# Performance work log

Hardware: AMD Instinct MI355X
Metric: run time of the kernel (lower is better)

## Reference

```python
import jax, jax.numpy as jnp
import numpy as np

N = 150000      # active voxels
C = 64          # head input channels
KK = 9          # 3x3 kernel offsets
H = W = 700     # BEV feature map
BN_EPS = 1e-5
HEADS = [("heatmap", 3), ("center", 2), ("center_z", 1), ("dim", 3), ("rot", 2)]


def _build_neighbor_table(seed=0):
    """Submanifold 3x3 neighbor indices for N active voxels on an HxW grid.
    Entry -1 means the neighbor site is inactive (contributes zero)."""
    rng = np.random.default_rng(seed)
    flat = rng.choice(H * W, size=N, replace=False)
    ys, xs = flat // W, flat % W
    lut = np.full(H * W, -1, np.int64)
    lut[flat] = np.arange(N)
    nbr = np.full((N, KK), -1, np.int64)
    k = 0
    for dy in (-1, 0, 1):
        for dx in (-1, 0, 1):
            ny, nx = ys + dy, xs + dx
            valid = (ny >= 0) & (ny < H) & (nx >= 0) & (nx < W)
            nf = np.where(valid, ny * W + nx, 0)
            nbr[:, k] = np.where(valid, lut[nf], -1)
            k += 1
    return nbr


def setup_inputs() -> dict:
    key = jax.random.key(0)
    ks = jax.random.split(key, 2 + 2 * len(HEADS))
    inp = {
        "features": jax.random.normal(ks[0], (N, C), jnp.float32),
        "nbr_idx": jnp.asarray(_build_neighbor_table(), jnp.int32),
        # one 3x3 subm conv per head, stacked: [n_heads, 9, C_in, C_out]
        "W3": jax.random.normal(ks[1], (len(HEADS), KK, C, C), jnp.float32) * 0.05,
        "gamma": jnp.ones((len(HEADS), C), jnp.float32),
        "beta": jnp.zeros((len(HEADS), C), jnp.float32),
    }
    for i, (name, oc) in enumerate(HEADS):
        inp[f"W1_{name}"] = jax.random.normal(ks[2 + i], (C, oc), jnp.float32) * 0.001
        if name == "heatmap":
            inp[f"b1_{name}"] = jnp.full((oc,), -float(np.log((1 - 0.01) / 0.01)), jnp.float32)
        else:
            inp[f"b1_{name}"] = jnp.zeros((oc,), jnp.float32)
    return inp


def _forward(features, nbr_idx, W3, gamma, beta, W1s, b1s):
    valid = nbr_idx >= 0                                  # [N, 9]
    idx = jnp.where(valid, nbr_idx, 0)
    # gather active-neighbor features; missing neighbors -> zero (subm conv)
    gathered = features[idx] * valid[..., None].astype(features.dtype)  # [N, 9, C]
    # all heads share the same input sparse tensor -> batched gather-GEMM
    h = jnp.einsum('nkc,hkco->hno', gathered, W3)         # [n_heads, N, C]
    # BatchNorm1d (training-mode batch stats, biased var) + ReLU
    mean = h.mean(axis=1, keepdims=True)
    var = ((h - mean) ** 2).mean(axis=1, keepdims=True)
    hn = (h - mean) * jax.lax.rsqrt(var + BN_EPS)
    hn = jax.nn.relu(hn * gamma[:, None, :] + beta[:, None, :])
    # per-head 1x1 subm conv == linear on active features
    return tuple(hn[i] @ W1s[i] + b1s[i] for i in range(len(HEADS)))


def reference(features, nbr_idx, W3, gamma, beta,
              W1_heatmap, b1_heatmap, W1_center, b1_center,
              W1_center_z, b1_center_z, W1_dim, b1_dim, W1_rot, b1_rot):
    W1s = [W1_heatmap, W1_center, W1_center_z, W1_dim, W1_rot]
    b1s = [b1_heatmap, b1_center, b1_center_z, b1_dim, b1_rot]
    return _forward(features, nbr_idx, W3, gamma, beta, W1s, b1s)
```

## Files before the change

### kernel.cpp

```cpp
#include <hip/hip_runtime.h>

#define NVOX 150000
#define BM 128
#define MTILES 1172
#define SROW 150016
#define NCOL 320

typedef __attribute__((ext_vector_type(8))) short bf16x8;
typedef __attribute__((ext_vector_type(4))) float f32x4;

__device__ __forceinline__ unsigned short f2bf(float f) {
    unsigned u = __builtin_bit_cast(unsigned, f);
    u += 0x7fffu + ((u >> 16) & 1u);
    return (unsigned short)(u >> 16);
}

__device__ __forceinline__ void gld16(const void* g, void* l) {
    __builtin_amdgcn_global_load_lds(
        (const __attribute__((address_space(1))) unsigned int*)g,
        (__attribute__((address_space(3))) unsigned int*)l, 16, 0, 0);
}

__global__ void prep_feat(const float* __restrict__ src, unsigned short* __restrict__ dst) {
    int i = blockIdx.x * 256 + threadIdx.x;
    if (i < NVOX * 64) dst[i] = f2bf(src[i]);
    else if (i < NVOX * 64 + 64) dst[i] = 0;
}

__global__ void prep_w3(const float* __restrict__ w3, unsigned short* __restrict__ bt,
                        float* __restrict__ stats) {
    int i = blockIdx.x * 256 + threadIdx.x;
    int h = i / 36864;
    int rem = i - h * 36864;
    int kk = rem >> 12;
    int c = (rem >> 6) & 63;
    int o = rem & 63;
    bt[(size_t)(((h * 9 + kk) * 8) + (c >> 3)) * 512 + o * 8 + (c & 7)] = f2bf(w3[i]);
    if (i < 2 * NCOL) stats[i] = 0.f;
}

__global__ __launch_bounds__(256, 4)
void gemm_kernel(const unsigned short* __restrict__ featB,
                 const unsigned short* __restrict__ Bt2,
                 const int* __restrict__ nbr,
                 unsigned short* __restrict__ hbuf,
                 float* __restrict__ stats) {
    __shared__ __align__(16) char smem[30208];
    constexpr int SB_OFF = 16384;
    constexpr int IDX_OFF = 24576;
    constexpr int SRED_OFF = 29184;

    int bid = blockIdx.x;
    int r = bid & 7, q = bid >> 3;
    int ntile = q % 5;
    int mtile = (q / 5) * 8 + r;
    if (mtile >= MTILES) return;
    int m0 = mtile * BM;
    int n0 = ntile * 64;

    int tid = threadIdx.x;
    int w = tid >> 6, lane = tid & 63;
    int quad = lane >> 4, m16 = lane & 15;

    for (int lin = tid; lin < BM * 9; lin += 256) {
        int row = lin / 9, kkq = lin - row * 9;
        int v = -1;
        if (m0 + row < NVOX) v = nbr[(size_t)(m0 + row) * 9 + kkq];
        *(int*)(smem + IDX_OFF + (kkq * BM + row) * 4) = ((v < 0) ? NVOX : v) * 128;
    }
    __syncthreads();

    f32x4 acc[4][2];
#pragma unroll
    for (int mt = 0; mt < 4; ++mt)
#pragma unroll
        for (int nt = 0; nt < 2; ++nt)
            acc[mt][nt] = (f32x4){0.f, 0.f, 0.f, 0.f};

    const char* fb = (const char*)featB;
    const char* bsrc = (const char*)Bt2 + (size_t)ntile * 73728;
    char* sA = smem;
    char* sB = smem + SB_OFF;

    int mrow = (w >> 1) * 64;
    int ncol = (w & 1) * 32;

    for (int kk = 0; kk < 9; ++kk) {
        int off0 = *(const int*)(smem + IDX_OFF + (kk * BM + lane) * 4);
        int off1 = *(const int*)(smem + IDX_OFF + (kk * BM + 64 + lane) * 4);
        int c16a = w * 2, c16b = w * 2 + 1;
        gld16(fb + off0 + c16a * 16, sA + c16a * 2048);
        gld16(fb + off1 + c16a * 16, sA + c16a * 2048 + 1024);
        gld16(fb + off0 + c16b * 16, sA + c16b * 2048);
        gld16(fb + off1 + c16b * 16, sA + c16b * 2048 + 1024);
        gld16(bsrc + (kk * 8 + c16a) * 1024 + lane * 16, sB + c16a * 1024);
        gld16(bsrc + (kk * 8 + c16b) * 1024 + lane * 16, sB + c16b * 1024);
        __syncthreads();
        bf16x8 af[2][4], bfr[2][2];
#pragma unroll
        for (int ks = 0; ks < 2; ++ks) {
#pragma unroll
            for (int mt = 0; mt < 4; ++mt)
                af[ks][mt] = *(const bf16x8*)(sA + (ks * 4 + quad) * 2048 +
                                              (mrow + mt * 16 + m16) * 16);
#pragma unroll
            for (int nt = 0; nt < 2; ++nt)
                bfr[ks][nt] = *(const bf16x8*)(sB + (ks * 4 + quad) * 1024 +
                                               (ncol + nt * 16 + m16) * 16);
        }
#pragma unroll
        for (int ks = 0; ks < 2; ++ks)
#pragma unroll
            for (int mt = 0; mt < 4; ++mt)
#pragma unroll
                for (int nt = 0; nt < 2; ++nt)
                    acc[mt][nt] = __builtin_amdgcn_mfma_f32_16x16x32_bf16(
                        af[ks][mt], bfr[ks][nt], acc[mt][nt], 0, 0, 0);
        __syncthreads();
    }

#pragma unroll
    for (int mt = 0; mt < 4; ++mt) {
#pragma unroll
        for (int nt = 0; nt < 2; ++nt) {
            int col = ncol + nt * 16 + m16;
            int row = mrow + mt * 16 + quad * 4;
            f32x4 v = acc[mt][nt];
            unsigned lo = (unsigned)f2bf(v.x) | ((unsigned)f2bf(v.y) << 16);
            unsigned hi = (unsigned)f2bf(v.z) | ((unsigned)f2bf(v.w) << 16);
            uint2 pk; pk.x = lo; pk.y = hi;
            *(uint2*)(smem + col * 272 + row * 2) = pk;
        }
    }
    __syncthreads();
#pragma unroll
    for (int it = 0; it < 8; ++it) {
        int col = it * 8 + (tid >> 5);
        int l32 = tid & 31;
        uint2 v = *(const uint2*)(smem + col * 272 + l32 * 8);
        *(uint2*)(hbuf + (size_t)(n0 + col) * SROW + m0 + l32 * 4) = v;
    }

    float s[2], ss[2];
#pragma unroll
    for (int nt = 0; nt < 2; ++nt) {
        float a = 0.f, b = 0.f;
#pragma unroll
        for (int mt = 0; mt < 4; ++mt) {
            f32x4 v = acc[mt][nt];
            a += v.x + v.y + v.z + v.w;
            b += v.x * v.x + v.y * v.y + v.z * v.z + v.w * v.w;
        }
        s[nt] = a; ss[nt] = b;
        s[nt] += __shfl_xor(s[nt], 16); s[nt] += __shfl_xor(s[nt], 32);
        ss[nt] += __shfl_xor(ss[nt], 16); ss[nt] += __shfl_xor(ss[nt], 32);
    }
    if (quad == 0) {
#pragma unroll
        for (int nt = 0; nt < 2; ++nt) {
            float* p = (float*)(smem + SRED_OFF + ((w * 2 + nt) * 16 + m16) * 8);
            p[0] = s[nt]; p[1] = ss[nt];
        }
    }
    __syncthreads();
    if (tid < 64) {
        int col = tid;
        int half = col >> 5, nt = (col >> 4) & 1, mc = col & 15;
        const float* p0 = (const float*)(smem + SRED_OFF + ((half * 2 + nt) * 16 + mc) * 8);
        const float* p1 = (const float*)(smem + SRED_OFF + (((2 + half) * 2 + nt) * 16 + mc) * 8);
        atomicAdd(&stats[n0 + col], p0[0] + p1[0]);
        atomicAdd(&stats[NCOL + n0 + col], p0[1] + p1[1]);
    }
}

__global__ void head_kernel(const unsigned short* __restrict__ hbuf,
                            const float* __restrict__ stats,
                            const float* __restrict__ gamma, const float* __restrict__ beta,
                            const float* __restrict__ W1_0, const float* __restrict__ W1_1,
                            const float* __restrict__ W1_2, const float* __restrict__ W1_3,
                            const float* __restrict__ W1_4,
                            const float* __restrict__ b1_0, const float* __restrict__ b1_1,
                            const float* __restrict__ b1_2, const float* __restrict__ b1_3,
                            const float* __restrict__ b1_4,
                            float* __restrict__ out) {
    __shared__ float sScale[NCOL], sShift[NCOL], sW1[NCOL * 3], sB1[16];
    int tid = threadIdx.x;
    for (int c = tid; c < NCOL; c += 256) {
        float mean = stats[c] * (1.f / (float)NVOX);
        float var = stats[NCOL + c] * (1.f / (float)NVOX) - mean * mean;
        float inv = rsqrtf(var + 1e-5f);
        float sc = inv * gamma[c];
        sScale[c] = sc;
        sShift[c] = beta[c] - mean * sc;
    }
    for (int i = tid; i < 192; i += 256) { int cc = i / 3, jj = i - cc * 3; sW1[0 * 192 + i] = W1_0[cc * 3 + jj]; }
    for (int i = tid; i < 192; i += 256) { int cc = i / 3, jj = i - cc * 3; sW1[1 * 192 + i] = (jj < 2) ? W1_1[cc * 2 + jj] : 0.f; }
    for (int i = tid; i < 192; i += 256) { int cc = i / 3, jj = i - cc * 3; sW1[2 * 192 + i] = (jj < 1) ? W1_2[cc] : 0.f; }
    for (int i = tid; i < 192; i += 256) { int cc = i / 3, jj = i - cc * 3; sW1[3 * 192 + i] = W1_3[cc * 3 + jj]; }
    for (int i = tid; i < 192; i += 256) { int cc = i / 3, jj = i - cc * 3; sW1[4 * 192 + i] = (jj < 2) ? W1_4[cc * 2 + jj] : 0.f; }
    if (tid == 0) {
        sB1[0] = b1_0[0]; sB1[1] = b1_0[1]; sB1[2] = b1_0[2];
        sB1[3] = b1_1[0]; sB1[4] = b1_1[1]; sB1[5] = 0.f;
        sB1[6] = b1_2[0]; sB1[7] = 0.f;    sB1[8] = 0.f;
        sB1[9] = b1_3[0]; sB1[10] = b1_3[1]; sB1[11] = b1_3[2];
        sB1[12] = b1_4[0]; sB1[13] = b1_4[1]; sB1[14] = 0.f;
    }
    __syncthreads();
    int n = 2 * (blockIdx.x * 256 + tid);
    if (n >= NVOX) return;
    const unsigned short* hp = hbuf + n;
#pragma unroll
    for (int h = 0; h < 5; ++h) {
        float x0 = sB1[h * 3 + 0], x1 = sB1[h * 3 + 1], x2 = sB1[h * 3 + 2];
        float y0 = x0, y1 = x1, y2 = x2;
#pragma unroll 8
        for (int cc = 0; cc < 64; ++cc) {
            int c = h * 64 + cc;
            unsigned raw = *(const unsigned*)(hp + (size_t)c * SROW);
            float v0 = __builtin_bit_cast(float, raw << 16);
            float v1 = __builtin_bit_cast(float, raw & 0xffff0000u);
            float sc = sScale[c], sh = sShift[c];
            v0 = fmaxf(v0 * sc + sh, 0.f);
            v1 = fmaxf(v1 * sc + sh, 0.f);
            float w0 = sW1[c * 3 + 0], w1 = sW1[c * 3 + 1], w2 = sW1[c * 3 + 2];
            x0 += v0 * w0; x1 += v0 * w1; x2 += v0 * w2;
            y0 += v1 * w0; y1 += v1 * w1; y2 += v1 * w2;
        }
        if (h == 0) {
            out[n * 3 + 0] = x0; out[n * 3 + 1] = x1; out[n * 3 + 2] = x2;
            out[(n + 1) * 3 + 0] = y0; out[(n + 1) * 3 + 1] = y1; out[(n + 1) * 3 + 2] = y2;
        } else if (h == 1) {
            out[450000 + n * 2 + 0] = x0; out[450000 + n * 2 + 1] = x1;
            out[450000 + (n + 1) * 2 + 0] = y0; out[450000 + (n + 1) * 2 + 1] = y1;
        } else if (h == 2) {
            out[750000 + n] = x0; out[750000 + n + 1] = y0;
        } else if (h == 3) {
            out[900000 + n * 3 + 0] = x0; out[900000 + n * 3 + 1] = x1; out[900000 + n * 3 + 2] = x2;
            out[900000 + (n + 1) * 3 + 0] = y0; out[900000 + (n + 1) * 3 + 1] = y1; out[900000 + (n + 1) * 3 + 2] = y2;
        } else {
            out[1350000 + n * 2 + 0] = x0; out[1350000 + n * 2 + 1] = x1;
            out[1350000 + (n + 1) * 2 + 0] = y0; out[1350000 + (n + 1) * 2 + 1] = y1;
        }
    }
}

extern "C" void kernel_launch(void* const* d_in, const int* in_sizes, int n_in,
                              void* d_out, int out_size, void* d_ws, size_t ws_size,
                              hipStream_t stream) {
    const float* features = (const float*)d_in[0];
    const int* nbr        = (const int*)d_in[1];
    const float* w3       = (const float*)d_in[2];
    const float* gamma    = (const float*)d_in[3];
    const float* beta     = (const float*)d_in[4];
    const float* W1_0 = (const float*)d_in[5];  const float* b1_0 = (const float*)d_in[6];
    const float* W1_1 = (const float*)d_in[7];  const float* b1_1 = (const float*)d_in[8];
    const float* W1_2 = (const float*)d_in[9];  const float* b1_2 = (const float*)d_in[10];
    const float* W1_3 = (const float*)d_in[11]; const float* b1_3 = (const float*)d_in[12];
    const float* W1_4 = (const float*)d_in[13]; const float* b1_4 = (const float*)d_in[14];
    float* out = (float*)d_out;

    char* ws = (char*)d_ws;
    unsigned short* featB = (unsigned short*)ws;
    unsigned short* Bt2   = (unsigned short*)(ws + 19200128);
    float* stats          = (float*)(ws + 19568768);
    unsigned short* hbuf  = (unsigned short*)(ws + 19571328);

    prep_feat<<<(NVOX * 64 + 64 + 255) / 256, 256, 0, stream>>>(features, featB);
    prep_w3<<<184320 / 256, 256, 0, stream>>>(w3, Bt2, stats);
    gemm_kernel<<<8 * 5 * 147, 256, 0, stream>>>(featB, Bt2, nbr, hbuf, stats);
    head_kernel<<<(NVOX / 2 + 255) / 256, 256, 0, stream>>>(hbuf, stats, gamma, beta,
        W1_0, W1_1, W1_2, W1_3, W1_4, b1_0, b1_1, b1_2, b1_3, b1_4, out);
}
```

Measured before the change: 228.4 us.

## Double-buffer gather-GEMM loads, vectorize feature prep, split head kernel per head

The gather-GEMM now double-buffers its A/B LDS tiles so the next kernel offset's global-to-LDS loads are issued before the current MFMAs, and it hoists the neighbor offsets into registers. This roughly doubles LDS use and lowers the occupancy target from 4 to 3 blocks. The bf16 conversion of features now handles 8 elements per thread with vector loads and stores. The head kernel is split across a 2D grid, one head per y-block, with 4 voxels per thread, which gives more parallelism and wider loads.

```diff
diff --git a/kernel.cpp b/kernel.cpp
--- a/kernel.cpp
+++ b/kernel.cpp
@@ -23,8 +23,18 @@
 
 __global__ void prep_feat(const float* __restrict__ src, unsigned short* __restrict__ dst) {
     int i = blockIdx.x * 256 + threadIdx.x;
-    if (i < NVOX * 64) dst[i] = f2bf(src[i]);
-    else if (i < NVOX * 64 + 64) dst[i] = 0;
+    if (i < NVOX * 8) {
+        const float* s = src + (size_t)i * 8;
+        float4 a = *(const float4*)s;
+        float4 b = *(const float4*)(s + 4);
+        union { bf16x8 v; unsigned short u[8]; } r;
+        r.u[0] = f2bf(a.x); r.u[1] = f2bf(a.y); r.u[2] = f2bf(a.z); r.u[3] = f2bf(a.w);
+        r.u[4] = f2bf(b.x); r.u[5] = f2bf(b.y); r.u[6] = f2bf(b.z); r.u[7] = f2bf(b.w);
+        *(bf16x8*)(dst + (size_t)i * 8) = r.v;
+    } else if (i < NVOX * 8 + 8) {
+        bf16x8 z = {0, 0, 0, 0, 0, 0, 0, 0};
+        *(bf16x8*)(dst + (size_t)i * 8) = z;
+    }
 }
 
 __global__ void prep_w3(const float* __restrict__ w3, unsigned short* __restrict__ bt,
@@ -39,16 +49,15 @@
     if (i < 2 * NCOL) stats[i] = 0.f;
 }
 
-__global__ __launch_bounds__(256, 4)
+__global__ __launch_bounds__(256, 3)
 void gemm_kernel(const unsigned short* __restrict__ featB,
                  const unsigned short* __restrict__ Bt2,
                  const int* __restrict__ nbr,
                  unsigned short* __restrict__ hbuf,
                  float* __restrict__ stats) {
-    __shared__ __align__(16) char smem[30208];
-    constexpr int SB_OFF = 16384;
-    constexpr int IDX_OFF = 24576;
-    constexpr int SRED_OFF = 29184;
+    __shared__ __align__(16) char smem[53760];
+    constexpr int IDX_OFF = 49152;
+    constexpr int SRED_OFF = 32768;
 
     int bid = blockIdx.x;
     int r = bid & 7, q = bid >> 3;
@@ -70,6 +79,13 @@
     }
     __syncthreads();
 
+    int off0r[9], off1r[9];
+#pragma unroll
+    for (int kk = 0; kk < 9; ++kk) {
+        off0r[kk] = *(const int*)(smem + IDX_OFF + (kk * BM + lane) * 4);
+        off1r[kk] = *(const int*)(smem + IDX_OFF + (kk * BM + 64 + lane) * 4);
+    }
+
     f32x4 acc[4][2];
 #pragma unroll
     for (int mt = 0; mt < 4; ++mt)
@@ -79,33 +95,40 @@
 
     const char* fb = (const char*)featB;
     const char* bsrc = (const char*)Bt2 + (size_t)ntile * 73728;
-    char* sA = smem;
-    char* sB = smem + SB_OFF;
+    char* sAb[2] = {smem, smem + 16384};
+    char* sBb[2] = {smem + 32768, smem + 40960};
 
     int mrow = (w >> 1) * 64;
     int ncol = (w & 1) * 32;
-
-    for (int kk = 0; kk < 9; ++kk) {
-        int off0 = *(const int*)(smem + IDX_OFF + (kk * BM + lane) * 4);
-        int off1 = *(const int*)(smem + IDX_OFF + (kk * BM + 64 + lane) * 4);
-        int c16a = w * 2, c16b = w * 2 + 1;
+    int c16a = w * 2, c16b = w * 2 + 1;
+
+    auto stage = [&](char* sA, char* sB, int kk, int off0, int off1) {
         gld16(fb + off0 + c16a * 16, sA + c16a * 2048);
         gld16(fb + off1 + c16a * 16, sA + c16a * 2048 + 1024);
         gld16(fb + off0 + c16b * 16, sA + c16b * 2048);
         gld16(fb + off1 + c16b * 16, sA + c16b * 2048 + 1024);
         gld16(bsrc + (kk * 8 + c16a) * 1024 + lane * 16, sB + c16a * 1024);
         gld16(bsrc + (kk * 8 + c16b) * 1024 + lane * 16, sB + c16b * 1024);
-        __syncthreads();
+    };
+
+    stage(sAb[0], sBb[0], 0, off0r[0], off1r[0]);
+    __syncthreads();
+
+#pragma unroll
+    for (int kk = 0; kk < 9; ++kk) {
+        const int cur = kk & 1;
+        if (kk < 8)
+            stage(sAb[cur ^ 1], sBb[cur ^ 1], kk + 1, off0r[kk + 1], off1r[kk + 1]);
         bf16x8 af[2][4], bfr[2][2];
 #pragma unroll
         for (int ks = 0; ks < 2; ++ks) {
 #pragma unroll
             for (int mt = 0; mt < 4; ++mt)
-                af[ks][mt] = *(const bf16x8*)(sA + (ks * 4 + quad) * 2048 +
+                af[ks][mt] = *(const bf16x8*)(sAb[cur] + (ks * 4 + quad) * 2048 +
                                               (mrow + mt * 16 + m16) * 16);
 #pragma unroll
             for (int nt = 0; nt < 2; ++nt)
-                bfr[ks][nt] = *(const bf16x8*)(sB + (ks * 4 + quad) * 1024 +
+                bfr[ks][nt] = *(const bf16x8*)(sBb[cur] + (ks * 4 + quad) * 1024 +
                                                (ncol + nt * 16 + m16) * 16);
         }
 #pragma unroll
@@ -173,74 +196,75 @@
     }
 }
 
-__global__ void head_kernel(const unsigned short* __restrict__ hbuf,
-                            const float* __restrict__ stats,
-                            const float* __restrict__ gamma, const float* __restrict__ beta,
-                            const float* __restrict__ W1_0, const float* __restrict__ W1_1,
-                            const float* __restrict__ W1_2, const float* __restrict__ W1_3,
-                            const float* __restrict__ W1_4,
-                            const float* __restrict__ b1_0, const float* __restrict__ b1_1,
-                            const float* __restrict__ b1_2, const float* __restrict__ b1_3,
-                            const float* __restrict__ b1_4,
-                            float* __restrict__ out) {
-    __shared__ float sScale[NCOL], sShift[NCOL], sW1[NCOL * 3], sB1[16];
+__global__ __launch_bounds__(256)
+void head_kernel(const unsigned short* __restrict__ hbuf,
+                 const float* __restrict__ stats,
+                 const float* __restrict__ gamma, const float* __restrict__ beta,
+                 const float* __restrict__ W1_0, const float* __restrict__ W1_1,
+                 const float* __restrict__ W1_2, const float* __restrict__ W1_3,
+                 const float* __restrict__ W1_4,
+                 const float* __restrict__ b1_0, const float* __restrict__ b1_1,
+                 const float* __restrict__ b1_2, const float* __restrict__ b1_3,
+                 const float* __restrict__ b1_4,
+                 float* __restrict__ out) {
+    __shared__ float sScale[64], sShift[64], sW1[192], sB1[3];
+    int h = blockIdx.y;
+    const float* W1; const float* b1; int oc; size_t obase;
+    if (h == 0)      { W1 = W1_0; b1 = b1_0; oc = 3; obase = 0; }
+    else if (h == 1) { W1 = W1_1; b1 = b1_1; oc = 2; obase = 450000; }
+    else if (h == 2) { W1 = W1_2; b1 = b1_2; oc = 1; obase = 750000; }
+    else if (h == 3) { W1 = W1_3; b1 = b1_3; oc = 3; obase = 900000; }
+    else             { W1 = W1_4; b1 = b1_4; oc = 2; obase = 1350000; }
+
     int tid = threadIdx.x;
-    for (int c = tid; c < NCOL; c += 256) {
+    if (tid < 64) {
+        int c = h * 64 + tid;
         float mean = stats[c] * (1.f / (float)NVOX);
         float var = stats[NCOL + c] * (1.f / (float)NVOX) - mean * mean;
         float inv = rsqrtf(var + 1e-5f);
         float sc = inv * gamma[c];
-        sScale[c] = sc;
-        sShift[c] = beta[c] - mean * sc;
-    }
-    for (int i = tid; i < 192; i += 256) { int cc = i / 3, jj = i - cc * 3; sW1[0 * 192 + i] = W1_0[cc * 3 + jj]; }
-    for (int i = tid; i < 192; i += 256) { int cc = i / 3, jj = i - cc * 3; sW1[1 * 192 + i] = (jj < 2) ? W1_1[cc * 2 + jj] : 0.f; }
-    for (int i = tid; i < 192; i += 256) { int cc = i / 3, jj = i - cc * 3; sW1[2 * 192 + i] = (jj < 1) ? W1_2[cc] : 0.f; }
-    for (int i = tid; i < 192; i += 256) { int cc = i / 3, jj = i - cc * 3; sW1[3 * 192 + i] = W1_3[cc * 3 + jj]; }
-    for (int i = tid; i < 192; i += 256) { int cc = i / 3, jj = i - cc * 3; sW1[4 * 192 + i] = (jj < 2) ? W1_4[cc * 2 + jj] : 0.f; }
+        sScale[tid] = sc;
+        sShift[tid] = beta[c] - mean * sc;
+    }
+    for (int i = tid; i < 192; i += 256) {
+        int cc = i / 3, jj = i - cc * 3;
+        sW1[i] = (jj < oc) ? W1[cc * oc + jj] : 0.f;
+    }
     if (tid == 0) {
-        sB1[0] = b1_0[0]; sB1[1] = b1_0[1]; sB1[2] = b1_0[2];
-        sB1[3] = b1_1[0]; sB1[4] = b1_1[1]; sB1[5] = 0.f;
-        sB1[6] = b1_2[0]; sB1[7] = 0.f;    sB1[8] = 0.f;
-        sB1[9] = b1_3[0]; sB1[10] = b1_3[1]; sB1[11] = b1_3[2];
-        sB1[12] = b1_4[0]; sB1[13] = b1_4[1]; sB1[14] = 0.f;
-    }
-    __syncthreads();
-    int n = 2 * (blockIdx.x * 256 + tid);
+        sB1[0] = b1[0];
+        sB1[1] = (oc >= 2) ? b1[1] : 0.f;
+        sB1[2] = (oc >= 3) ? b1[2] : 0.f;
+    }
+    __syncthreads();
+
+    int n = (blockIdx.x * 256 + tid) * 4;
     if (n >= NVOX) return;
-    const unsigned short* hp = hbuf + n;
-#pragma unroll
-    for (int h = 0; h < 5; ++h) {
-        float x0 = sB1[h * 3 + 0], x1 = sB1[h * 3 + 1], x2 = sB1[h * 3 + 2];
-        float y0 = x0, y1 = x1, y2 = x2;
+    const unsigned short* hp = hbuf + (size_t)(h * 64) * SROW + n;
+    float x[4][3];
+#pragma unroll
+    for (int rr = 0; rr < 4; ++rr) { x[rr][0] = sB1[0]; x[rr][1] = sB1[1]; x[rr][2] = sB1[2]; }
 #pragma unroll 8
-        for (int cc = 0; cc < 64; ++cc) {
-            int c = h * 64 + cc;
-            unsigned raw = *(const unsigned*)(hp + (size_t)c * SROW);
-            float v0 = __builtin_bit_cast(float, raw << 16);
-            float v1 = __builtin_bit_cast(float, raw & 0xffff0000u);
-            float sc = sScale[c], sh = sShift[c];
-            v0 = fmaxf(v0 * sc + sh, 0.f);
-            v1 = fmaxf(v1 * sc + sh, 0.f);
-            float w0 = sW1[c * 3 + 0], w1 = sW1[c * 3 + 1], w2 = sW1[c * 3 + 2];
-            x0 += v0 * w0; x1 += v0 * w1; x2 += v0 * w2;
-            y0 += v1 * w0; y1 += v1 * w1; y2 += v1 * w2;
-        }
-        if (h == 0) {
-            out[n * 3 + 0] = x0; out[n * 3 + 1] = x1; out[n * 3 + 2] = x2;
-            out[(n + 1) * 3 + 0] = y0; out[(n + 1) * 3 + 1] = y1; out[(n + 1) * 3 + 2] = y2;
-        } else if (h == 1) {
-            out[450000 + n * 2 + 0] = x0; out[450000 + n * 2 + 1] = x1;
-            out[450000 + (n + 1) * 2 + 0] = y0; out[450000 + (n + 1) * 2 + 1] = y1;
-        } else if (h == 2) {
-            out[750000 + n] = x0; out[750000 + n + 1] = y0;
-        } else if (h == 3) {
-            out[900000 + n * 3 + 0] = x0; out[900000 + n * 3 + 1] = x1; out[900000 + n * 3 + 2] = x2;
-            out[900000 + (n + 1) * 3 + 0] = y0; out[900000 + (n + 1) * 3 + 1] = y1; out[900000 + (n + 1) * 3 + 2] = y2;
-        } else {
-            out[1350000 + n * 2 + 0] = x0; out[1350000 + n * 2 + 1] = x1;
-            out[1350000 + (n + 1) * 2 + 0] = y0; out[1350000 + (n + 1) * 2 + 1] = y1;
-        }
+    for (int cc = 0; cc < 64; ++cc) {
+        uint2 raw = *(const uint2*)(hp + (size_t)cc * SROW);
+        float sc = sScale[cc], sh = sShift[cc];
+        float w0 = sW1[cc * 3 + 0], w1 = sW1[cc * 3 + 1], w2 = sW1[cc * 3 + 2];
+        float v0 = __builtin_bit_cast(float, raw.x << 16);
+        float v1 = __builtin_bit_cast(float, raw.x & 0xffff0000u);
+        float v2 = __builtin_bit_cast(float, raw.y << 16);
+        float v3 = __builtin_bit_cast(float, raw.y & 0xffff0000u);
+        v0 = fmaxf(v0 * sc + sh, 0.f); v1 = fmaxf(v1 * sc + sh, 0.f);
+        v2 = fmaxf(v2 * sc + sh, 0.f); v3 = fmaxf(v3 * sc + sh, 0.f);
+        x[0][0] += v0 * w0; x[0][1] += v0 * w1; x[0][2] += v0 * w2;
+        x[1][0] += v1 * w0; x[1][1] += v1 * w1; x[1][2] += v1 * w2;
+        x[2][0] += v2 * w0; x[2][1] += v2 * w1; x[2][2] += v2 * w2;
+        x[3][0] += v3 * w0; x[3][1] += v3 * w1; x[3][2] += v3 * w2;
+    }
+#pragma unroll
+    for (int rr = 0; rr < 4; ++rr) {
+        float* op = out + obase + (size_t)(n + rr) * oc;
+        op[0] = x[rr][0];
+        if (oc >= 2) op[1] = x[rr][1];
+        if (oc >= 3) op[2] = x[rr][2];
     }
 }
 
@@ -265,9 +289,9 @@
     float* stats          = (float*)(ws + 19568768);
     unsigned short* hbuf  = (unsigned short*)(ws + 19571328);
 
-    prep_feat<<<(NVOX * 64 + 64 + 255) / 256, 256, 0, stream>>>(features, featB);
+    prep_feat<<<(NVOX * 8 + 8 + 255) / 256, 256, 0, stream>>>(features, featB);
     prep_w3<<<184320 / 256, 256, 0, stream>>>(w3, Bt2, stats);
     gemm_kernel<<<8 * 5 * 147, 256, 0, stream>>>(featB, Bt2, nbr, hbuf, stats);
-    head_kernel<<<(NVOX / 2 + 255) / 256, 256, 0, stream>>>(hbuf, stats, gamma, beta,
+    head_kernel<<<dim3(147, 5), 256, 0, stream>>>(hbuf, stats, gamma, beta,
         W1_0, W1_1, W1_2, W1_3, W1_4, b1_0, b1_1, b1_2, b1_3, b1_4, out);
 }
```

Result: no change. 224.7 us (-1.6%).
